# Kernel optimization log

Hardware: AMD Instinct MI355X
Metric: run time of the kernel (lower is better)

The kernel has to match this reference:

```python
import jax, jax.numpy as jnp
import numpy as np

DIM = 1024
H = 8
HK = DIM // H  # head key dim = 128 (expand_k=1.0)
HV = DIM // H  # head value dim = 128 (expand_v=1.0)
GLR = 16       # gate low-rank dim (fla default)
GATE_LOGIT_NORMALIZER = 16.0
EPS = 1e-5
B, T = 2, 512


def setup_inputs() -> dict:
    key = jax.random.key(0)
    ks = jax.random.split(key, 9)
    s = lambda k, shp: jax.random.normal(k, shp, jnp.float32) * (shp[0] ** -0.5)
    return {
        "x": jax.random.normal(ks[0], (B, T, DIM), jnp.float32),
        "Wq": s(ks[1], (DIM, DIM)),
        "Wk": s(ks[2], (DIM, DIM)),
        "Wv": s(ks[3], (DIM, DIM)),
        "Wg": s(ks[4], (DIM, DIM)),
        "Wgk1": s(ks[5], (DIM, GLR)),
        "Wgk2": s(ks[6], (GLR, DIM)),
        "bgk2": jnp.zeros((DIM,), jnp.float32),
        "g_norm_w": jnp.ones((HV,), jnp.float32),
        "Wo": s(ks[7], (DIM, DIM)),
    }


def _gla_forward(x, Wq, Wk, Wv, Wg, Wgk1, Wgk2, bgk2, g_norm_w, Wo):
    b, t, _ = x.shape
    # projections
    q = (x @ Wq).reshape(b, t, H, HK) * (HK ** -0.5)
    k = (x @ Wk).reshape(b, t, H, HK)
    v = (x @ Wv).reshape(b, t, H, HV)
    # low-rank forget gate: logsigmoid / normalizer, per key channel
    gk = (jax.nn.log_sigmoid((x @ Wgk1) @ Wgk2 + bgk2) / GATE_LOGIT_NORMALIZER)
    gk = gk.reshape(b, t, H, HK)

    # recurrent decay-gated linear attention:
    #   S_t = diag(exp(gk_t)) @ S_{t-1} + k_t^T v_t ; o_t = q_t @ S_t
    def step(h, inp):
        qt, kt, vt, gt = inp  # each [B, H, HK] / [B, H, HV]
        h = h * jnp.exp(gt)[..., None] + kt[..., None] * vt[..., None, :]
        ot = jnp.einsum("bhk,bhkv->bhv", qt, h)
        return h, ot

    h0 = jnp.zeros((b, H, HK, HV), x.dtype)
    xs = (
        q.transpose(1, 0, 2, 3),
        k.transpose(1, 0, 2, 3),
        v.transpose(1, 0, 2, 3),
        gk.transpose(1, 0, 2, 3),
    )
    _, o = jax.lax.scan(step, h0, xs)  # o: [T, B, H, HV]
    o = o.transpose(1, 0, 2, 3)        # [B, T, H, HV]

    # gated RMSNorm with swish gate over per-head value dim, then output proj
    g = (x @ Wg).reshape(b, t, H, HV)
    rms = jax.lax.rsqrt(jnp.mean(o * o, axis=-1, keepdims=True) + EPS)
    o = (o * rms) * g_norm_w * (g * jax.nn.sigmoid(g))
    return o.reshape(b, t, DIM) @ Wo


def reference(x, Wq, Wk, Wv, Wg, Wgk1, Wgk2, bgk2, g_norm_w, Wo):
    return _gla_forward(x, Wq, Wk, Wv, Wg, Wgk1, Wgk2, bgk2, g_norm_w, Wo)
```

## Files before the change

kernel.cpp:

```cpp
#include <hip/hip_runtime.h>
#include <hip/hip_bf16.h>
#include <math.h>

#define BT     1024
#define NH     8
#define SEGLEN 32
#define NSEG   16
#define NBH    16
#define QKS    136
#define VTS    40
#define AMS    40

typedef __attribute__((ext_vector_type(8))) short short8;
typedef __attribute__((ext_vector_type(4))) short sh4;
typedef __attribute__((ext_vector_type(4))) float f32x4;

__device__ __forceinline__ float bitf(short u) {
    union { float f; unsigned i; } x; x.i = ((unsigned)(unsigned short)u) << 16; return x.f;
}
__device__ __forceinline__ short f2bf(float f) {
    union { float f; unsigned u; } x; x.f = f;
    unsigned r = x.u + 0x7FFF + ((x.u >> 16) & 1);
    return (short)(r >> 16);
}
__device__ __forceinline__ void gload_lds16(const short* g, short* l) {
    __builtin_amdgcn_global_load_lds(
        (const __attribute__((address_space(1))) unsigned int*)g,
        (__attribute__((address_space(3))) unsigned int*)l, 16, 0, 0);
}

__global__ __launch_bounds__(256) void cast_all(
    const float* __restrict__ Wq, const float* __restrict__ Wk,
    const float* __restrict__ Wv, const float* __restrict__ Wg,
    const float* __restrict__ Wo, const float* __restrict__ X,
    const float* __restrict__ Wgk1,
    short* __restrict__ WT, short* __restrict__ Xb, short* __restrict__ Wgk1T)
{
    const int z = blockIdx.z;
    const int tid = threadIdx.x;
    if (z == 5) {
        const int id = blockIdx.y * 32 + blockIdx.x;
        const int i = id * 1024 + tid * 4;
        float4 a = *(const float4*)(X + i);
        sh4 v;
        v[0] = f2bf(a.x); v[1] = f2bf(a.y); v[2] = f2bf(a.z); v[3] = f2bf(a.w);
        *(sh4*)(Xb + i) = v;
        return;
    }
    if (z == 6) {
        const int id = blockIdx.y * 32 + blockIdx.x;
        if (id >= 16) return;
        const int d = id * 64 + (tid & 63), jj = tid >> 6;
        float4 w = *(const float4*)(Wgk1 + d * 16 + jj * 4);
        Wgk1T[(jj * 4 + 0) * 1024 + d] = f2bf(w.x);
        Wgk1T[(jj * 4 + 1) * 1024 + d] = f2bf(w.y);
        Wgk1T[(jj * 4 + 2) * 1024 + d] = f2bf(w.z);
        Wgk1T[(jj * 4 + 3) * 1024 + d] = f2bf(w.w);
        return;
    }
    const float* W = (z == 0) ? Wq : (z == 1) ? Wk : (z == 2) ? Wv : (z == 3) ? Wg : Wo;
    short* T = WT + (size_t)z * (1u << 20);
    __shared__ float tile[32][33];
    const int k0 = blockIdx.y * 32, n0 = blockIdx.x * 32;
    const int row = tid >> 3, c4 = (tid & 7) << 2;
    float4 f = *(const float4*)(W + (size_t)(k0 + row) * 1024 + n0 + c4);
    tile[row][c4 + 0] = f.x; tile[row][c4 + 1] = f.y;
    tile[row][c4 + 2] = f.z; tile[row][c4 + 3] = f.w;
    __syncthreads();
    short* o = T + (size_t)(n0 + row) * 1024 + k0 + c4;
    o[0] = f2bf(tile[c4 + 0][row]); o[1] = f2bf(tile[c4 + 1][row]);
    o[2] = f2bf(tile[c4 + 2][row]); o[3] = f2bf(tile[c4 + 3][row]);
}

__global__ __launch_bounds__(256) void proj_gemm(
    const short* __restrict__ Xb, const short* __restrict__ WT,
    short* __restrict__ QKVG)
{
    const int z = blockIdx.z;
    const float scale = (z == 0) ? 0.08838834764831845f : 1.0f;
    short* C = QKVG + (size_t)z * (1u << 20);
    const short* B = WT + (size_t)z * (1u << 20);

    __shared__ __align__(16) short As[8 * 64 * 8];
    __shared__ __align__(16) short Bs[8 * 128 * 8];
    const int tid = threadIdx.x;
    const int wave = tid >> 6, lane = tid & 63;
    const int wm = (wave >> 1) * 32, wn = (wave & 1) * 64;
    const int m15 = lane & 15, q = lane >> 4;
    const int m0 = blockIdx.y * 64, n0 = blockIdx.x * 128;

    f32x4 acc[2][4];
    #pragma unroll
    for (int i = 0; i < 2; i++)
        #pragma unroll
        for (int j = 0; j < 4; j++)
            acc[i][j] = (f32x4){0.f, 0.f, 0.f, 0.f};

    for (int kb0 = 0; kb0 < 1024; kb0 += 64) {
        __syncthreads();
        #pragma unroll
        for (int c = 0; c < 2; c++) {
            const int k8 = wave * 2 + c;
            gload_lds16(Xb + (size_t)(m0 + lane) * 1024 + kb0 + k8 * 8,
                        &As[(k8 * 64) * 8]);
            #pragma unroll
            for (int rh = 0; rh < 2; rh++)
                gload_lds16(B + (size_t)(n0 + rh * 64 + lane) * 1024 + kb0 + k8 * 8,
                            &Bs[(k8 * 128 + rh * 64) * 8]);
        }
        __syncthreads();
        #pragma unroll
        for (int s = 0; s < 2; s++) {
            const int k8 = s * 4 + q;
            short8 af[2], bf[4];
            #pragma unroll
            for (int i = 0; i < 2; i++)
                af[i] = *(const short8*)&As[(k8 * 64 + wm + i * 16 + m15) * 8];
            #pragma unroll
            for (int j = 0; j < 4; j++)
                bf[j] = *(const short8*)&Bs[(k8 * 128 + wn + j * 16 + m15) * 8];
            #pragma unroll
            for (int i = 0; i < 2; i++)
                #pragma unroll
                for (int j = 0; j < 4; j++)
                    acc[i][j] = __builtin_amdgcn_mfma_f32_16x16x32_bf16(af[i], bf[j], acc[i][j], 0, 0, 0);
        }
    }
    #pragma unroll
    for (int i = 0; i < 2; i++)
        #pragma unroll
        for (int j = 0; j < 4; j++)
            #pragma unroll
            for (int rr = 0; rr < 4; rr++)
                C[(size_t)(m0 + wm + i * 16 + q * 4 + rr) * 1024 + n0 + wn + j * 16 + m15] =
                    f2bf(acc[i][j][rr] * scale);
}

__global__ __launch_bounds__(256) void wo_gemm(
    const short* __restrict__ A, const short* __restrict__ B, float* __restrict__ C)
{
    __shared__ __align__(16) short As[8 * 64 * 8];
    __shared__ __align__(16) short Bs[8 * 64 * 8];
    const int tid = threadIdx.x;
    const int wave = tid >> 6, lane = tid & 63;
    const int wm = (wave >> 1) * 32, wn = (wave & 1) * 32;
    const int m15 = lane & 15, q = lane >> 4;
    const int m0 = blockIdx.y * 64, n0 = blockIdx.x * 64;

    f32x4 acc[2][2];
    #pragma unroll
    for (int i = 0; i < 2; i++)
        #pragma unroll
        for (int j = 0; j < 2; j++)
            acc[i][j] = (f32x4){0.f, 0.f, 0.f, 0.f};

    for (int kb0 = 0; kb0 < 1024; kb0 += 64) {
        __syncthreads();
        #pragma unroll
        for (int c = 0; c < 2; c++) {
            const int k8 = wave * 2 + c;
            gload_lds16(A + (size_t)(m0 + lane) * 1024 + kb0 + k8 * 8, &As[(k8 * 64) * 8]);
            gload_lds16(B + (size_t)(n0 + lane) * 1024 + kb0 + k8 * 8, &Bs[(k8 * 64) * 8]);
        }
        __syncthreads();
        #pragma unroll
        for (int s = 0; s < 2; s++) {
            const int k8 = s * 4 + q;
            short8 af[2], bf[2];
            #pragma unroll
            for (int i = 0; i < 2; i++)
                af[i] = *(const short8*)&As[(k8 * 64 + wm + i * 16 + m15) * 8];
            #pragma unroll
            for (int j = 0; j < 2; j++)
                bf[j] = *(const short8*)&Bs[(k8 * 64 + wn + j * 16 + m15) * 8];
            #pragma unroll
            for (int i = 0; i < 2; i++)
                #pragma unroll
                for (int j = 0; j < 2; j++)
                    acc[i][j] = __builtin_amdgcn_mfma_f32_16x16x32_bf16(af[i], bf[j], acc[i][j], 0, 0, 0);
        }
    }
    #pragma unroll
    for (int i = 0; i < 2; i++)
        #pragma unroll
        for (int j = 0; j < 2; j++)
            #pragma unroll
            for (int rr = 0; rr < 4; rr++)
                C[(size_t)(m0 + wm + i * 16 + q * 4 + rr) * 1024 + n0 + wn + j * 16 + m15] =
                    acc[i][j][rr];
}

__global__ __launch_bounds__(256) void gk_proj(
    const short* __restrict__ Xb, const short* __restrict__ Wgk1T,
    const float* __restrict__ Wgk2, const float* __restrict__ bgk2,
    short* __restrict__ GK)
{
    const int row = blockIdx.x, tid = threadIdx.x;
    const int d4 = tid * 4;
    sh4 xv = *(const sh4*)(Xb + (size_t)row * 1024 + d4);
    float x0 = bitf(xv[0]), x1 = bitf(xv[1]), x2 = bitf(xv[2]), x3 = bitf(xv[3]);
    float p[16];
    #pragma unroll
    for (int j = 0; j < 16; j++) {
        sh4 w = *(const sh4*)(Wgk1T + j * 1024 + d4);
        p[j] = x0 * bitf(w[0]) + x1 * bitf(w[1]) + x2 * bitf(w[2]) + x3 * bitf(w[3]);
    }
    #pragma unroll
    for (int j = 0; j < 16; j++)
        #pragma unroll
        for (int off = 32; off; off >>= 1) p[j] += __shfl_xor(p[j], off);
    __shared__ float zp[4][16];
    __shared__ float z[16];
    const int lane = tid & 63, w = tid >> 6;
    if (lane == 0) {
        #pragma unroll
        for (int j = 0; j < 16; j++) zp[w][j] = p[j];
    }
    __syncthreads();
    if (tid < 16) z[tid] = zp[0][tid] + zp[1][tid] + zp[2][tid] + zp[3][tid];
    __syncthreads();
    for (int c = tid; c < 1024; c += 256) {
        float acc = bgk2[c];
        #pragma unroll
        for (int j = 0; j < 16; j++)
            acc = fmaf(z[j], Wgk2[j * 1024 + c], acc);
        float ls = fminf(acc, 0.f) - log1pf(expf(-fabsf(acc)));
        GK[(size_t)row * 1024 + c] = f2bf(ls * (1.f / 16.f));
    }
}

__global__ __launch_bounds__(256) void scan_chunk(
    const short* __restrict__ Q, const short* __restrict__ K,
    const short* __restrict__ V, short* GKQT,
    short* __restrict__ O, short* __restrict__ SS, float* __restrict__ DSEG)
{
    const int seg = blockIdx.x;
    const int bh  = blockIdx.y;
    const int b = bh >> 3, h = bh & 7;
    const int tid = threadIdx.x;
    const int wave = tid >> 6, lane = tid & 63;
    const size_t rowbase = (size_t)(b * 512 + seg * SEGLEN) * 1024 + h * 128;

    __shared__ __align__(16) short Qt[32 * QKS];
    __shared__ __align__(16) short Kt[32 * QKS];
    __shared__ __align__(16) short Vs[32 * 128];
    __shared__ __align__(16) short VT[128 * VTS];
    __shared__ __align__(16) short KhT[128 * VTS];
    __shared__ __align__(16) short Am[32 * AMS];
    __shared__ float htot[2][128];

    #pragma unroll
    for (int c = 0; c < 2; c++) {
        const int fb = (wave * 2 + c) * 64;
        const int f = fb + lane;
        const int t = f >> 4, c8 = f & 15;
        gload_lds16(V + rowbase + (size_t)t * 1024 + c8 * 8, &Vs[fb * 8]);
    }

    const int ch = tid & 127, th2 = tid >> 7;
    float g[16], kv[16], qv[16];
    #pragma unroll
    for (int tt = 0; tt < 16; tt++) {
        const size_t a = rowbase + (size_t)(th2 * 16 + tt) * 1024 + ch;
        g[tt] = bitf(GKQT[a]); kv[tt] = bitf(K[a]); qv[tt] = bitf(Q[a]);
    }
    float run = 0.f;
    #pragma unroll
    for (int tt = 0; tt < 16; tt++) { run += g[tt]; g[tt] = run; }
    htot[th2][ch] = run;
    __syncthreads();
    const float base_ = th2 ? htot[0][ch] : 0.f;
    const float eGend = expf(htot[0][ch] + htot[1][ch]);
    if (th2 == 0) DSEG[(bh * NSEG + seg) * 128 + ch] = eGend;
    #pragma unroll
    for (int tt = 0; tt < 16; tt++) {
        const int t = th2 * 16 + tt;
        const size_t a = rowbase + (size_t)t * 1024 + ch;
        const float Gc = base_ + g[tt];
        const float eg = expf(Gc);
        short qts = f2bf(qv[tt] * eg);
        Qt[t * QKS + ch] = qts;
        GKQT[a] = qts;
        float ktv = kv[tt] * expf(-Gc);
        Kt[t * QKS + ch] = f2bf(ktv);
        KhT[ch * VTS + t] = f2bf(ktv * eGend);
    }
    __syncthreads();
    {
        const int vch = tid >> 1, t0 = (tid & 1) * 16;
        #pragma unroll
        for (int j = 0; j < 4; j++) {
            sh4 p;
            p[0] = Vs[(t0 + 4 * j + 0) * 128 + vch];
            p[1] = Vs[(t0 + 4 * j + 1) * 128 + vch];
            p[2] = Vs[(t0 + 4 * j + 2) * 128 + vch];
            p[3] = Vs[(t0 + 4 * j + 3) * 128 + vch];
            *(sh4*)&VT[vch * VTS + t0 + 4 * j] = p;
        }
    }
    __syncthreads();

    const int m15 = lane & 15, q = lane >> 4;

    {
        const int mi = wave >> 1, ni = wave & 1;
        f32x4 a1 = (f32x4){0.f, 0.f, 0.f, 0.f};
        #pragma unroll
        for (int kc = 0; kc < 4; kc++) {
            short8 af = *(const short8*)&Qt[(mi * 16 + m15) * QKS + kc * 32 + q * 8];
            short8 bf = *(const short8*)&Kt[(ni * 16 + m15) * QKS + kc * 32 + q * 8];
            a1 = __builtin_amdgcn_mfma_f32_16x16x32_bf16(af, bf, a1, 0, 0, 0);
        }
        #pragma unroll
        for (int rr = 0; rr < 4; rr++) {
            const int t = mi * 16 + q * 4 + rr, s = ni * 16 + m15;
            Am[t * AMS + s] = (t >= s) ? f2bf(a1[rr]) : (short)0;
        }
    }
    __syncthreads();

    {
        const int mi = wave >> 1, nb = (wave & 1) * 4;
        short8 af = *(const short8*)&Am[(mi * 16 + m15) * AMS + q * 8];
        #pragma unroll
        for (int jj = 0; jj < 4; jj++) {
            short8 bf = *(const short8*)&VT[((nb + jj) * 16 + m15) * VTS + q * 8];
            f32x4 a2 = (f32x4){0.f, 0.f, 0.f, 0.f};
            a2 = __builtin_amdgcn_mfma_f32_16x16x32_bf16(af, bf, a2, 0, 0, 0);
            #pragma unroll
            for (int rr = 0; rr < 4; rr++)
                O[rowbase + (size_t)(mi * 16 + q * 4 + rr) * 1024 + (nb + jj) * 16 + m15] =
                    f2bf(a2[rr]);
        }
    }

    {
        const size_t sbase = (size_t)(bh * NSEG + seg) * 16384;
        #pragma unroll
        for (int m2 = 0; m2 < 2; m2++) {
            const int mrow = wave * 2 + m2;
            short8 af = *(const short8*)&VT[(mrow * 16 + m15) * VTS + q * 8];
            #pragma unroll
            for (int ni = 0; ni < 8; ni++) {
                short8 bf = *(const short8*)&KhT[(ni * 16 + m15) * VTS + q * 8];
                f32x4 a3 = (f32x4){0.f, 0.f, 0.f, 0.f};
                a3 = __builtin_amdgcn_mfma_f32_16x16x32_bf16(af, bf, a3, 0, 0, 0);
                #pragma unroll
                for (int rr = 0; rr < 4; rr++)
                    SS[sbase + (size_t)(mrow * 16 + q * 4 + rr) * 128 + ni * 16 + m15] =
                        f2bf(a3[rr]);
            }
        }
    }
}

__global__ __launch_bounds__(256) void stitch(
    short* __restrict__ SS, const float* __restrict__ DSEG)
{
    const int slice = blockIdx.x;
    const int bh = blockIdx.y, tid = threadIdx.x;
    __shared__ float dloc[NSEG][128];
    for (int i = tid; i < NSEG * 128; i += 256)
        dloc[i >> 7][i & 127] = DSEG[(bh * NSEG + (i >> 7)) * 128 + (i & 127)];
    __syncthreads();
    const int kch0 = (tid * 2) & 127;
    float run[2][2] = {{0.f, 0.f}, {0.f, 0.f}};
    for (int seg = 0; seg < NSEG; seg++) {
        const size_t base = (size_t)(bh * NSEG + seg) * 16384 + slice * 1024;
        const float d0 = dloc[seg][kch0], d1 = dloc[seg][kch0 + 1];
        #pragma unroll
        for (int j = 0; j < 2; j++) {
            unsigned* p = (unsigned*)&SS[base + j * 512 + tid * 2];
            unsigned u = *p;
            float t0 = bitf((short)(u & 0xFFFF));
            float t1 = bitf((short)(u >> 16));
            unsigned w0 = (unsigned short)f2bf(run[j][0]);
            unsigned w1 = (unsigned short)f2bf(run[j][1]);
            *p = w0 | (w1 << 16);
            run[j][0] = fmaf(run[j][0], d0, t0);
            run[j][1] = fmaf(run[j][1], d1, t1);
        }
    }
}

__global__ __launch_bounds__(256) void corr_gnorm(
    const short* __restrict__ QT, const short* __restrict__ SS,
    const short* __restrict__ O, const short* __restrict__ G,
    const float* __restrict__ gnw, short* __restrict__ Obf)
{
    const int seg = blockIdx.x;
    const int bh = blockIdx.y;
    const int b = bh >> 3, h = bh & 7;
    const int tid = threadIdx.x;
    const int wave = tid >> 6, lane = tid & 63;
    const int m15 = lane & 15, q = lane >> 4;
    const size_t rowbase = (size_t)(b * 512 + seg * SEGLEN) * 1024 + h * 128;
    const size_t sbase = (size_t)(bh * NSEG + seg) * 16384;

    __shared__ __align__(16) short Qs[16 * 32 * 8];
    __shared__ __align__(16) short Ss[16 * 128 * 8];
    __shared__ __align__(16) short Gs[16 * 32 * 8];
    __shared__ __align__(16) short Os[16 * 32 * 8];
    __shared__ float red[4][16];

    #pragma unroll
    for (int c = 0; c < 2; c++) {
        const int fb = (wave * 2 + c) * 64;
        const int f = fb + lane;
        const int k8 = f >> 5, t = f & 31;
        gload_lds16(QT + rowbase + (size_t)t * 1024 + k8 * 8, &Qs[fb * 8]);
    }
    #pragma unroll
    for (int c = 0; c < 2; c++) {
        const int fb = (wave * 2 + c) * 64;
        const int f = fb + lane;
        const int v8 = f >> 5, t = f & 31;
        gload_lds16(G + rowbase + (size_t)t * 1024 + v8 * 8, &Gs[fb * 8]);
        gload_lds16(O + rowbase + (size_t)t * 1024 + v8 * 8, &Os[fb * 8]);
    }
    #pragma unroll
    for (int c = 0; c < 8; c++) {
        const int fb = wave * 512 + c * 64;
        const int f = fb + lane;
        const int k8 = f >> 7, vch = f & 127;
        gload_lds16(SS + sbase + (size_t)vch * 128 + k8 * 8, &Ss[fb * 8]);
    }
    __syncthreads();

    const int mt = wave >> 1, nh2 = wave & 1;
    f32x4 acc[4];
    #pragma unroll
    for (int nt = 0; nt < 4; nt++) acc[nt] = (f32x4){0.f, 0.f, 0.f, 0.f};
    #pragma unroll
    for (int kb = 0; kb < 4; kb++) {
        short8 af = *(const short8*)&Qs[((kb * 4 + q) * 32 + mt * 16 + m15) * 8];
        #pragma unroll
        for (int nt = 0; nt < 4; nt++) {
            short8 bf = *(const short8*)&Ss[((kb * 4 + q) * 128 + nh2 * 64 + nt * 16 + m15) * 8];
            acc[nt] = __builtin_amdgcn_mfma_f32_16x16x32_bf16(af, bf, acc[nt], 0, 0, 0);
        }
    }

    float o[4][4];
    float ssq[4] = {0.f, 0.f, 0.f, 0.f};
    #pragma unroll
    for (int nt = 0; nt < 4; nt++) {
        const int vch = nh2 * 64 + nt * 16 + m15;
        #pragma unroll
        for (int rr = 0; rr < 4; rr++) {
            const int t = mt * 16 + q * 4 + rr;
            float ov = bitf(Os[((vch >> 3) * 32 + t) * 8 + (vch & 7)]) + acc[nt][rr];
            o[nt][rr] = ov;
            ssq[rr] = fmaf(ov, ov, ssq[rr]);
        }
    }
    #pragma unroll
    for (int rr = 0; rr < 4; rr++) {
        ssq[rr] += __shfl_xor(ssq[rr], 1);
        ssq[rr] += __shfl_xor(ssq[rr], 2);
        ssq[rr] += __shfl_xor(ssq[rr], 4);
        ssq[rr] += __shfl_xor(ssq[rr], 8);
    }
    if (m15 == 0) {
        #pragma unroll
        for (int rr = 0; rr < 4; rr++) red[wave][q * 4 + rr] = ssq[rr];
    }
    __syncthreads();
    float rsq[4];
    #pragma unroll
    for (int rr = 0; rr < 4; rr++) {
        float ms = (red[wave][q * 4 + rr] + red[wave ^ 1][q * 4 + rr]) * (1.f / 128.f);
        rsq[rr] = rsqrtf(ms + 1e-5f);
    }
    #pragma unroll
    for (int nt = 0; nt < 4; nt++) {
        const int vch = nh2 * 64 + nt * 16 + m15;
        const float gw = gnw[vch];
        #pragma unroll
        for (int rr = 0; rr < 4; rr++) {
            const int t = mt * 16 + q * 4 + rr;
            float g = bitf(Gs[((vch >> 3) * 32 + t) * 8 + (vch & 7)]);
            float sg = g / (1.f + expf(-g));
            Obf[rowbase + (size_t)t * 1024 + vch] = f2bf(o[nt][rr] * rsq[rr] * gw * sg);
        }
    }
}

extern "C" void kernel_launch(void* const* d_in, const int* in_sizes, int n_in,
                              void* d_out, int out_size, void* d_ws, size_t ws_size,
                              hipStream_t stream)
{
    const float* X    = (const float*)d_in[0];
    const float* Wq   = (const float*)d_in[1];
    const float* Wk   = (const float*)d_in[2];
    const float* Wv   = (const float*)d_in[3];
    const float* Wg   = (const float*)d_in[4];
    const float* Wgk1 = (const float*)d_in[5];
    const float* Wgk2 = (const float*)d_in[6];
    const float* bgk2 = (const float*)d_in[7];
    const float* gnw  = (const float*)d_in[8];
    const float* Wo   = (const float*)d_in[9];
    float* OUT = (float*)d_out;

    short* QKVG  = (short*)d_ws;
    short* GK    = QKVG + (4u << 20);
    short* Ob    = GK + (1u << 20);
    short* SS    = Ob + (1u << 20);
    float* DS    = (float*)(SS + (4u << 20));
    short* WT    = (short*)(DS + 32768);
    short* Xb    = WT + (5u << 20);
    short* Wgk1T = Xb + (1u << 20);
    short* Obf   = QKVG;

    cast_all<<<dim3(32, 32, 7), 256, 0, stream>>>(Wq, Wk, Wv, Wg, Wo, X, Wgk1, WT, Xb, Wgk1T);
    proj_gemm<<<dim3(8, 16, 4), 256, 0, stream>>>(Xb, WT, QKVG);
    gk_proj<<<dim3(BT), 256, 0, stream>>>(Xb, Wgk1T, Wgk2, bgk2, GK);
    scan_chunk<<<dim3(NSEG, NBH), 256, 0, stream>>>(
        QKVG, QKVG + (1u << 20), QKVG + (2u << 20), GK, Ob, SS, DS);
    stitch<<<dim3(16, NBH), 256, 0, stream>>>(SS, DS);
    corr_gnorm<<<dim3(NSEG, NBH), 256, 0, stream>>>(
        GK, SS, Ob, QKVG + (3u << 20), gnw, Obf);
    wo_gemm<<<dim3(16, 16), 256, 0, stream>>>(Obf, WT + (4u << 20), OUT);
}
```

Baseline: 158.4 us.

## Fuse chunk scan, state stitch and correction/gnorm into one cooperative kernel

Merges the three chunk-scan, stitch and correction/gated-RMSNorm kernels into a single cooperative kernel, using grid.sync between phases. The intra-chunk output stays in registers and the decayed Q stays in shared memory across the syncs, so they are no longer written to and re-read from global memory. A shared-memory union lets the phases reuse the same space. This removes two kernel launches and some global traffic, but adds two grid-wide barriers and needs all 256 blocks to be resident at the same time.

```diff
diff --git a/kernel.cpp b/kernel.cpp
--- a/kernel.cpp
+++ b/kernel.cpp
@@ -1,5 +1,6 @@
 #include <hip/hip_runtime.h>
 #include <hip/hip_bf16.h>
+#include <hip/hip_cooperative_groups.h>
 #include <math.h>
 
 #define BT     1024
@@ -229,61 +230,72 @@
     }
 }
 
-__global__ __launch_bounds__(256) void scan_chunk(
+__global__ __launch_bounds__(256) void scan_mega(
     const short* __restrict__ Q, const short* __restrict__ K,
-    const short* __restrict__ V, short* GKQT,
-    short* __restrict__ O, short* __restrict__ SS, float* __restrict__ DSEG)
+    const short* __restrict__ V, const short* __restrict__ GK,
+    const short* __restrict__ G, const float* __restrict__ gnw,
+    short* __restrict__ SS, float* __restrict__ DSEG, short* __restrict__ Obf)
 {
+    cooperative_groups::grid_group grid = cooperative_groups::this_grid();
     const int seg = blockIdx.x;
     const int bh  = blockIdx.y;
     const int b = bh >> 3, h = bh & 7;
     const int tid = threadIdx.x;
     const int wave = tid >> 6, lane = tid & 63;
+    const int m15 = lane & 15, q = lane >> 4;
     const size_t rowbase = (size_t)(b * 512 + seg * SEGLEN) * 1024 + h * 128;
+    const size_t sbase = (size_t)(bh * NSEG + seg) * 16384;
 
     __shared__ __align__(16) short Qt[32 * QKS];
-    __shared__ __align__(16) short Kt[32 * QKS];
-    __shared__ __align__(16) short Vs[32 * 128];
-    __shared__ __align__(16) short VT[128 * VTS];
-    __shared__ __align__(16) short KhT[128 * VTS];
-    __shared__ __align__(16) short Am[32 * AMS];
-    __shared__ float htot[2][128];
+    __shared__ __align__(16) union {
+        struct {
+            short Kt[32 * QKS];
+            short Vs[32 * 128];
+            short VT[128 * VTS];
+            short KhT[128 * VTS];
+            short Am[32 * AMS];
+            float htot[2][128];
+        } s;
+        struct {
+            short Ss[16 * 128 * 8];
+            short Gs[16 * 32 * 8];
+            float red[4][16];
+            float dloc[NSEG][128];
+        } c;
+    } u;
 
     #pragma unroll
     for (int c = 0; c < 2; c++) {
         const int fb = (wave * 2 + c) * 64;
         const int f = fb + lane;
         const int t = f >> 4, c8 = f & 15;
-        gload_lds16(V + rowbase + (size_t)t * 1024 + c8 * 8, &Vs[fb * 8]);
-    }
-
+        gload_lds16(V + rowbase + (size_t)t * 1024 + c8 * 8, &u.s.Vs[fb * 8]);
+    }
     const int ch = tid & 127, th2 = tid >> 7;
-    float g[16], kv[16], qv[16];
-    #pragma unroll
-    for (int tt = 0; tt < 16; tt++) {
-        const size_t a = rowbase + (size_t)(th2 * 16 + tt) * 1024 + ch;
-        g[tt] = bitf(GKQT[a]); kv[tt] = bitf(K[a]); qv[tt] = bitf(Q[a]);
-    }
-    float run = 0.f;
-    #pragma unroll
-    for (int tt = 0; tt < 16; tt++) { run += g[tt]; g[tt] = run; }
-    htot[th2][ch] = run;
-    __syncthreads();
-    const float base_ = th2 ? htot[0][ch] : 0.f;
-    const float eGend = expf(htot[0][ch] + htot[1][ch]);
-    if (th2 == 0) DSEG[(bh * NSEG + seg) * 128 + ch] = eGend;
-    #pragma unroll
-    for (int tt = 0; tt < 16; tt++) {
-        const int t = th2 * 16 + tt;
-        const size_t a = rowbase + (size_t)t * 1024 + ch;
-        const float Gc = base_ + g[tt];
-        const float eg = expf(Gc);
-        short qts = f2bf(qv[tt] * eg);
-        Qt[t * QKS + ch] = qts;
-        GKQT[a] = qts;
-        float ktv = kv[tt] * expf(-Gc);
-        Kt[t * QKS + ch] = f2bf(ktv);
-        KhT[ch * VTS + t] = f2bf(ktv * eGend);
+    {
+        float g[16], kv[16], qv[16];
+        #pragma unroll
+        for (int tt = 0; tt < 16; tt++) {
+            const size_t a = rowbase + (size_t)(th2 * 16 + tt) * 1024 + ch;
+            g[tt] = bitf(GK[a]); kv[tt] = bitf(K[a]); qv[tt] = bitf(Q[a]);
+        }
+        float run = 0.f;
+        #pragma unroll
+        for (int tt = 0; tt < 16; tt++) { run += g[tt]; g[tt] = run; }
+        u.s.htot[th2][ch] = run;
+        __syncthreads();
+        const float base_ = th2 ? u.s.htot[0][ch] : 0.f;
+        const float eGend = expf(u.s.htot[0][ch] + u.s.htot[1][ch]);
+        if (th2 == 0) DSEG[(bh * NSEG + seg) * 128 + ch] = eGend;
+        #pragma unroll
+        for (int tt = 0; tt < 16; tt++) {
+            const int t = th2 * 16 + tt;
+            const float Gc = base_ + g[tt];
+            Qt[t * QKS + ch] = f2bf(qv[tt] * expf(Gc));
+            float ktv = kv[tt] * expf(-Gc);
+            u.s.Kt[t * QKS + ch] = f2bf(ktv);
+            u.s.KhT[ch * VTS + t] = f2bf(ktv * eGend);
+        }
     }
     __syncthreads();
     {
@@ -291,16 +303,14 @@
         #pragma unroll
         for (int j = 0; j < 4; j++) {
             sh4 p;
-            p[0] = Vs[(t0 + 4 * j + 0) * 128 + vch];
-            p[1] = Vs[(t0 + 4 * j + 1) * 128 + vch];
-            p[2] = Vs[(t0 + 4 * j + 2) * 128 + vch];
-            p[3] = Vs[(t0 + 4 * j + 3) * 128 + vch];
-            *(sh4*)&VT[vch * VTS + t0 + 4 * j] = p;
-        }
-    }
-    __syncthreads();
-
-    const int m15 = lane & 15, q = lane >> 4;
+            p[0] = u.s.Vs[(t0 + 4 * j + 0) * 128 + vch];
+            p[1] = u.s.Vs[(t0 + 4 * j + 1) * 128 + vch];
+            p[2] = u.s.Vs[(t0 + 4 * j + 2) * 128 + vch];
+            p[3] = u.s.Vs[(t0 + 4 * j + 3) * 128 + vch];
+            *(sh4*)&u.s.VT[vch * VTS + t0 + 4 * j] = p;
+        }
+    }
+    __syncthreads();
 
     {
         const int mi = wave >> 1, ni = wave & 1;
@@ -308,41 +318,37 @@
         #pragma unroll
         for (int kc = 0; kc < 4; kc++) {
             short8 af = *(const short8*)&Qt[(mi * 16 + m15) * QKS + kc * 32 + q * 8];
-            short8 bf = *(const short8*)&Kt[(ni * 16 + m15) * QKS + kc * 32 + q * 8];
+            short8 bf = *(const short8*)&u.s.Kt[(ni * 16 + m15) * QKS + kc * 32 + q * 8];
             a1 = __builtin_amdgcn_mfma_f32_16x16x32_bf16(af, bf, a1, 0, 0, 0);
         }
         #pragma unroll
         for (int rr = 0; rr < 4; rr++) {
             const int t = mi * 16 + q * 4 + rr, s = ni * 16 + m15;
-            Am[t * AMS + s] = (t >= s) ? f2bf(a1[rr]) : (short)0;
-        }
-    }
-    __syncthreads();
-
+            u.s.Am[t * AMS + s] = (t >= s) ? f2bf(a1[rr]) : (short)0;
+        }
+    }
+    __syncthreads();
+
+    f32x4 o_i[4];
     {
         const int mi = wave >> 1, nb = (wave & 1) * 4;
-        short8 af = *(const short8*)&Am[(mi * 16 + m15) * AMS + q * 8];
+        short8 af = *(const short8*)&u.s.Am[(mi * 16 + m15) * AMS + q * 8];
         #pragma unroll
         for (int jj = 0; jj < 4; jj++) {
-            short8 bf = *(const short8*)&VT[((nb + jj) * 16 + m15) * VTS + q * 8];
+            short8 bf = *(const short8*)&u.s.VT[((nb + jj) * 16 + m15) * VTS + q * 8];
             f32x4 a2 = (f32x4){0.f, 0.f, 0.f, 0.f};
-            a2 = __builtin_amdgcn_mfma_f32_16x16x32_bf16(af, bf, a2, 0, 0, 0);
-            #pragma unroll
-            for (int rr = 0; rr < 4; rr++)
-                O[rowbase + (size_t)(mi * 16 + q * 4 + rr) * 1024 + (nb + jj) * 16 + m15] =
-                    f2bf(a2[rr]);
-        }
-    }
-
-    {
-        const size_t sbase = (size_t)(bh * NSEG + seg) * 16384;
+            o_i[jj] = __builtin_amdgcn_mfma_f32_16x16x32_bf16(af, bf, a2, 0, 0, 0);
+        }
+    }
+
+    {
         #pragma unroll
         for (int m2 = 0; m2 < 2; m2++) {
             const int mrow = wave * 2 + m2;
-            short8 af = *(const short8*)&VT[(mrow * 16 + m15) * VTS + q * 8];
+            short8 af = *(const short8*)&u.s.VT[(mrow * 16 + m15) * VTS + q * 8];
             #pragma unroll
             for (int ni = 0; ni < 8; ni++) {
-                short8 bf = *(const short8*)&KhT[(ni * 16 + m15) * VTS + q * 8];
+                short8 bf = *(const short8*)&u.s.KhT[(ni * 16 + m15) * VTS + q * 8];
                 f32x4 a3 = (f32x4){0.f, 0.f, 0.f, 0.f};
                 a3 = __builtin_amdgcn_mfma_f32_16x16x32_bf16(af, bf, a3, 0, 0, 0);
                 #pragma unroll
@@ -352,78 +358,49 @@
             }
         }
     }
-}
-
-__global__ __launch_bounds__(256) void stitch(
-    short* __restrict__ SS, const float* __restrict__ DSEG)
-{
-    const int slice = blockIdx.x;
-    const int bh = blockIdx.y, tid = threadIdx.x;
-    __shared__ float dloc[NSEG][128];
-    for (int i = tid; i < NSEG * 128; i += 256)
-        dloc[i >> 7][i & 127] = DSEG[(bh * NSEG + (i >> 7)) * 128 + (i & 127)];
-    __syncthreads();
-    const int kch0 = (tid * 2) & 127;
-    float run[2][2] = {{0.f, 0.f}, {0.f, 0.f}};
-    for (int seg = 0; seg < NSEG; seg++) {
-        const size_t base = (size_t)(bh * NSEG + seg) * 16384 + slice * 1024;
-        const float d0 = dloc[seg][kch0], d1 = dloc[seg][kch0 + 1];
-        #pragma unroll
-        for (int j = 0; j < 2; j++) {
-            unsigned* p = (unsigned*)&SS[base + j * 512 + tid * 2];
-            unsigned u = *p;
-            float t0 = bitf((short)(u & 0xFFFF));
-            float t1 = bitf((short)(u >> 16));
-            unsigned w0 = (unsigned short)f2bf(run[j][0]);
-            unsigned w1 = (unsigned short)f2bf(run[j][1]);
-            *p = w0 | (w1 << 16);
-            run[j][0] = fmaf(run[j][0], d0, t0);
-            run[j][1] = fmaf(run[j][1], d1, t1);
-        }
-    }
-}
-
-__global__ __launch_bounds__(256) void corr_gnorm(
-    const short* __restrict__ QT, const short* __restrict__ SS,
-    const short* __restrict__ O, const short* __restrict__ G,
-    const float* __restrict__ gnw, short* __restrict__ Obf)
-{
-    const int seg = blockIdx.x;
-    const int bh = blockIdx.y;
-    const int b = bh >> 3, h = bh & 7;
-    const int tid = threadIdx.x;
-    const int wave = tid >> 6, lane = tid & 63;
-    const int m15 = lane & 15, q = lane >> 4;
-    const size_t rowbase = (size_t)(b * 512 + seg * SEGLEN) * 1024 + h * 128;
-    const size_t sbase = (size_t)(bh * NSEG + seg) * 16384;
-
-    __shared__ __align__(16) short Qs[16 * 32 * 8];
-    __shared__ __align__(16) short Ss[16 * 128 * 8];
-    __shared__ __align__(16) short Gs[16 * 32 * 8];
-    __shared__ __align__(16) short Os[16 * 32 * 8];
-    __shared__ float red[4][16];
-
-    #pragma unroll
-    for (int c = 0; c < 2; c++) {
-        const int fb = (wave * 2 + c) * 64;
+
+    grid.sync();
+
+    {
+        const int slice = blockIdx.x;
+        for (int i = tid; i < NSEG * 128; i += 256)
+            u.c.dloc[i >> 7][i & 127] = DSEG[(bh * NSEG + (i >> 7)) * 128 + (i & 127)];
+        __syncthreads();
+        const int kch0 = (tid * 2) & 127;
+        float run[2][2] = {{0.f, 0.f}, {0.f, 0.f}};
+        for (int sg = 0; sg < NSEG; sg++) {
+            const size_t base = (size_t)(bh * NSEG + sg) * 16384 + slice * 1024;
+            const float d0 = u.c.dloc[sg][kch0], d1 = u.c.dloc[sg][kch0 + 1];
+            #pragma unroll
+            for (int j = 0; j < 2; j++) {
+                unsigned* p = (unsigned*)&SS[base + j * 512 + tid * 2];
+                unsigned uu = *p;
+                float t0 = bitf((short)(uu & 0xFFFF));
+                float t1 = bitf((short)(uu >> 16));
+                unsigned w0 = (unsigned short)f2bf(run[j][0]);
+                unsigned w1 = (unsigned short)f2bf(run[j][1]);
+                *p = w0 | (w1 << 16);
+                run[j][0] = fmaf(run[j][0], d0, t0);
+                run[j][1] = fmaf(run[j][1], d1, t1);
+            }
+        }
+    }
+
+    grid.sync();
+
+    #pragma unroll
+    for (int c = 0; c < 8; c++) {
+        const int fb = wave * 512 + c * 64;
         const int f = fb + lane;
-        const int k8 = f >> 5, t = f & 31;
-        gload_lds16(QT + rowbase + (size_t)t * 1024 + k8 * 8, &Qs[fb * 8]);
+        const int k8 = f >> 7, vch = f & 127;
+        gload_lds16(SS + sbase + (size_t)vch * 128 + k8 * 8, &u.c.Ss[fb * 8]);
     }
     #pragma unroll
     for (int c = 0; c < 2; c++) {
         const int fb = (wave * 2 + c) * 64;
         const int f = fb + lane;
         const int v8 = f >> 5, t = f & 31;
-        gload_lds16(G + rowbase + (size_t)t * 1024 + v8 * 8, &Gs[fb * 8]);
-        gload_lds16(O + rowbase + (size_t)t * 1024 + v8 * 8, &Os[fb * 8]);
-    }
-    #pragma unroll
-    for (int c = 0; c < 8; c++) {
-        const int fb = wave * 512 + c * 64;
-        const int f = fb + lane;
-        const int k8 = f >> 7, vch = f & 127;
-        gload_lds16(SS + sbase + (size_t)vch * 128 + k8 * 8, &Ss[fb * 8]);
+        gload_lds16(G + rowbase + (size_t)t * 1024 + v8 * 8, &u.c.Gs[fb * 8]);
     }
     __syncthreads();
 
@@ -433,10 +410,10 @@
     for (int nt = 0; nt < 4; nt++) acc[nt] = (f32x4){0.f, 0.f, 0.f, 0.f};
     #pragma unroll
     for (int kb = 0; kb < 4; kb++) {
-        short8 af = *(const short8*)&Qs[((kb * 4 + q) * 32 + mt * 16 + m15) * 8];
+        short8 af = *(const short8*)&Qt[(mt * 16 + m15) * QKS + (kb * 4 + q) * 8];
         #pragma unroll
         for (int nt = 0; nt < 4; nt++) {
-            short8 bf = *(const short8*)&Ss[((kb * 4 + q) * 128 + nh2 * 64 + nt * 16 + m15) * 8];
+            short8 bf = *(const short8*)&u.c.Ss[((kb * 4 + q) * 128 + nh2 * 64 + nt * 16 + m15) * 8];
             acc[nt] = __builtin_amdgcn_mfma_f32_16x16x32_bf16(af, bf, acc[nt], 0, 0, 0);
         }
     }
@@ -445,11 +422,9 @@
     float ssq[4] = {0.f, 0.f, 0.f, 0.f};
     #pragma unroll
     for (int nt = 0; nt < 4; nt++) {
-        const int vch = nh2 * 64 + nt * 16 + m15;
         #pragma unroll
         for (int rr = 0; rr < 4; rr++) {
-            const int t = mt * 16 + q * 4 + rr;
-            float ov = bitf(Os[((vch >> 3) * 32 + t) * 8 + (vch & 7)]) + acc[nt][rr];
+            float ov = o_i[nt][rr] + acc[nt][rr];
             o[nt][rr] = ov;
             ssq[rr] = fmaf(ov, ov, ssq[rr]);
         }
@@ -463,13 +438,13 @@
     }
     if (m15 == 0) {
         #pragma unroll
-        for (int rr = 0; rr < 4; rr++) red[wave][q * 4 + rr] = ssq[rr];
+        for (int rr = 0; rr < 4; rr++) u.c.red[wave][q * 4 + rr] = ssq[rr];
     }
     __syncthreads();
     float rsq[4];
     #pragma unroll
     for (int rr = 0; rr < 4; rr++) {
-        float ms = (red[wave][q * 4 + rr] + red[wave ^ 1][q * 4 + rr]) * (1.f / 128.f);
+        float ms = (u.c.red[wave][q * 4 + rr] + u.c.red[wave ^ 1][q * 4 + rr]) * (1.f / 128.f);
         rsq[rr] = rsqrtf(ms + 1e-5f);
     }
     #pragma unroll
@@ -479,7 +454,7 @@
         #pragma unroll
         for (int rr = 0; rr < 4; rr++) {
             const int t = mt * 16 + q * 4 + rr;
-            float g = bitf(Gs[((vch >> 3) * 32 + t) * 8 + (vch & 7)]);
+            float g = bitf(u.c.Gs[((vch >> 3) * 32 + t) * 8 + (vch & 7)]);
             float sg = g / (1.f + expf(-g));
             Obf[rowbase + (size_t)t * 1024 + vch] = f2bf(o[nt][rr] * rsq[rr] * gw * sg);
         }
@@ -515,10 +490,17 @@
     cast_all<<<dim3(32, 32, 7), 256, 0, stream>>>(Wq, Wk, Wv, Wg, Wo, X, Wgk1, WT, Xb, Wgk1T);
     proj_gemm<<<dim3(8, 16, 4), 256, 0, stream>>>(Xb, WT, QKVG);
     gk_proj<<<dim3(BT), 256, 0, stream>>>(Xb, Wgk1T, Wgk2, bgk2, GK);
-    scan_chunk<<<dim3(NSEG, NBH), 256, 0, stream>>>(
-        QKVG, QKVG + (1u << 20), QKVG + (2u << 20), GK, Ob, SS, DS);
-    stitch<<<dim3(16, NBH), 256, 0, stream>>>(SS, DS);
-    corr_gnorm<<<dim3(NSEG, NBH), 256, 0, stream>>>(
-        GK, SS, Ob, QKVG + (3u << 20), gnw, Obf);
+    {
+        const short* Qc  = QKVG;
+        const short* Kc  = QKVG + (1u << 20);
+        const short* Vc  = QKVG + (2u << 20);
+        const short* GKc = GK;
+        const short* Gc  = QKVG + (3u << 20);
+        const float* gw  = gnw;
+        short* SSc = SS; float* DSc = DS; short* Oc = Obf;
+        void* args[] = {&Qc, &Kc, &Vc, &GKc, &Gc, &gw, &SSc, &DSc, &Oc};
+        hipLaunchCooperativeKernel((void*)scan_mega, dim3(NSEG, NBH), dim3(256),
+                                   args, 0, stream);
+    }
     wo_gemm<<<dim3(16, 16), 256, 0, stream>>>(Obf, WT + (4u << 20), OUT);
 }
```

New measurement: 239.6 us. 1.51x slower.
